# Kernel tuning notes

Measured on AMD Instinct MI355X. Metric: run time of the kernel, lower is better.

Reference implementation:

```python
import jax, jax.numpy as jnp
import numpy as np

N = 128   # system size (number of sequential RNN steps)
B = 8192  # batch of samples
H = 128   # hidden units per layer (units=[128,128])
D = 2     # input_dim (spin up/down one-hot)


def setup_inputs() -> dict:
    key = jax.random.key(0)
    ks = jax.random.split(key, 11)
    s = 1.0 / np.sqrt(H)  # torch nn.RNNCell/Linear default U(-1/sqrt(H), 1/sqrt(H))
    bits = jax.random.randint(ks[0], (N, B), 0, D)
    samples = jax.nn.one_hot(bits, D, dtype=jnp.float32)  # (N, B, D) one-hot spins
    u = lambda k, shp: jax.random.uniform(k, shp, jnp.float32, -s, s)
    return {
        "samples": samples,
        "W_ih0": u(ks[1], (H, D)), "b_ih0": u(ks[2], (H,)),
        "W_hh0": u(ks[3], (H, H)), "b_hh0": u(ks[4], (H,)),
        "W_ih1": u(ks[5], (H, H)), "b_ih1": u(ks[6], (H,)),
        "W_hh1": u(ks[7], (H, H)), "b_hh1": u(ks[8], (H,)),
        "W_dense": u(ks[9], (D, H)), "b_dense": u(ks[10], (D,)),
    }


def reference(samples, W_ih0, b_ih0, W_hh0, b_hh0,
              W_ih1, b_ih1, W_hh1, b_hh1, W_dense, b_dense):
    # Faithful jax port of RNN_wavefunction.log_prob:
    # p_t = <softmax(dense(h1_t)), s_t>; returns sum_t log p_t with shape (1, B).
    # For one-hot s_t, log(sum(prob*s_t)) == sum(s_t * log_softmax(logits)) (stable form).
    Bsz = samples.shape[1]
    # input at step t is the sampled spin from step t-1; zeros at t=0
    inputs = jnp.concatenate(
        [jnp.zeros((1, Bsz, D), samples.dtype), samples[:-1]], axis=0)
    h0 = jnp.zeros((Bsz, H), samples.dtype)
    h1 = jnp.zeros((Bsz, H), samples.dtype)

    def step(carry, xs):
        h0, h1 = carry
        x_t, s_t = xs  # x_t: (B, D) prev spin one-hot, s_t: (B, D) current spin
        # nn.RNNCell: h' = tanh(x W_ih^T + b_ih + h W_hh^T + b_hh)
        h0 = jnp.tanh(x_t @ W_ih0.T + b_ih0 + h0 @ W_hh0.T + b_hh0)
        h1 = jnp.tanh(h0 @ W_ih1.T + b_ih1 + h1 @ W_hh1.T + b_hh1)
        logits = h1 @ W_dense.T + b_dense           # (B, 2)
        logp = jax.nn.log_softmax(logits, axis=-1)
        lp_t = jnp.sum(logp * s_t, axis=-1)          # (B,) = log p(s_t)
        return (h0, h1), lp_t

    _, lps = jax.lax.scan(step, (h0, h1), (inputs, samples))  # lps: (N, B)
    return jnp.sum(lps, axis=0, keepdims=True)  # (1, B), matches torch keepdim=True
```

## Files before the change

### kernel.cpp

```cpp
#include <hip/hip_runtime.h>
#include <hip/hip_bf16.h>


#define NSTEP 128
#define BTOT  8192
#define HID   128
#define MB    16
#define NBLK  (BTOT / MB)
#define NTHR  256

typedef __attribute__((ext_vector_type(8))) short bf16x8;
typedef __attribute__((ext_vector_type(4))) float f32x4;

__device__ __forceinline__ short f2bf(float v) {
    unsigned u = __builtin_bit_cast(unsigned, v);
    u += 0x7FFFu + ((u >> 16) & 1u);
    return (short)(u >> 16);
}
__device__ __forceinline__ unsigned pk2bf(float a, float b) {
    unsigned ua = __builtin_bit_cast(unsigned, a);
    unsigned ub = __builtin_bit_cast(unsigned, b);
    ua += 0x7FFFu + ((ua >> 16) & 1u);
    ub += 0x7FFFu + ((ub >> 16) & 1u);
    return (ua >> 16) | (ub & 0xFFFF0000u);
}
__device__ __forceinline__ float fast_tanh(float x) {
    float e = __builtin_exp2f(x * 2.885390081777927f);
    float r = __builtin_amdgcn_rcpf(e + 1.0f);
    return 1.0f - 2.0f * r;
}

__global__ __launch_bounds__(NTHR, 2) void rnn_wf_kernel(
    const float* __restrict__ samples,
    const float* __restrict__ Wih0,
    const float* __restrict__ bih0,
    const float* __restrict__ Whh0,
    const float* __restrict__ bhh0,
    const float* __restrict__ Wih1,
    const float* __restrict__ bih1,
    const float* __restrict__ Whh1,
    const float* __restrict__ bhh1,
    const float* __restrict__ Wd,
    const float* __restrict__ bd,
    float* __restrict__ out)
{
    __shared__ short sH0[2][MB * HID];
    __shared__ short sH1[2][MB * HID];
    __shared__ unsigned sMask[NSTEP];

    const int tid  = threadIdx.x;
    const int b0   = blockIdx.x * MB;
    const int w    = tid >> 6;
    const int lane = tid & 63;
    const int q    = lane >> 4;
    const int c    = lane & 15;
    const int nb   = w * 32;

    for (int i = tid; i < MB * HID; i += NTHR) {
        sH0[0][i] = 0;
        sH1[0][i] = 0;
    }
    if (tid < NSTEP) {
        unsigned msk = 0;
        #pragma unroll
        for (int m = 0; m < MB; ++m) {
            float e1 = samples[((size_t)tid * BTOT + b0 + m) * 2 + 1];
            if (e1 > 0.5f) msk |= (1u << m);
        }
        sMask[tid] = msk;
    }

    bf16x8 fhh0[2][4], fih1[2][4], fhh1[2][4];
    #pragma unroll
    for (int nt = 0; nt < 2; ++nt) {
        const int nn = nb + nt * 16 + c;
        #pragma unroll
        for (int kb = 0; kb < 4; ++kb) {
            const int off = nn * HID + kb * 32 + q * 8;
            bf16x8 v0, v1, v2;
            #pragma unroll
            for (int j = 0; j < 8; ++j) {
                v0[j] = f2bf(Whh0[off + j]);
                v1[j] = f2bf(Wih1[off + j]);
                v2[j] = f2bf(Whh1[off + j]);
            }
            fhh0[nt][kb] = v0; fih1[nt][kb] = v1; fhh1[nt][kb] = v2;
        }
    }
    bf16x8 fwd[4];
    #pragma unroll
    for (int kb = 0; kb < 4; ++kb) {
        bf16x8 v;
        #pragma unroll
        for (int j = 0; j < 8; ++j)
            v[j] = (c < 2) ? f2bf(Wd[c * HID + kb * 32 + q * 8 + j]) : (short)0;
        fwd[kb] = v;
    }
    float pA[2][4], pB[2][4], b0v[2][4], b1v[2][4];
    #pragma unroll
    for (int nt = 0; nt < 2; ++nt)
        #pragma unroll
        for (int r = 0; r < 4; ++r) {
            const int n = nb + nt * 16 + q * 4 + r;
            const float bb = bih0[n] + bhh0[n];
            b0v[nt][r] = bb;
            pA[nt][r]  = bb + Wih0[n * 2 + 0];
            pB[nt][r]  = bb + Wih0[n * 2 + 1];
            b1v[nt][r] = bih1[n] + bhh1[n];
        }
    const float bd0 = bd[0], bd1 = bd[1];

    int ra[4];
    #pragma unroll
    for (int kb = 0; kb < 4; ++kb)
        ra[kb] = c * HID + (((kb * 4 + q) ^ (c & 7)) << 3);
    int wa[2];
    #pragma unroll
    for (int nt = 0; nt < 2; ++nt)
        wa[nt] = c * HID + ((((w << 2) + (nt << 1) + (q >> 1)) ^ (c & 7)) << 3)
               + ((q & 1) << 2);

    __syncthreads();

    float lp = 0.0f;
    int cur = 0;

    for (int t = 0; t < NSTEP; ++t) {
        const short* h0c = sH0[cur];
        short*       h0n = sH0[cur ^ 1];
        const short* h1c = sH1[cur];
        short*       h1n = sH1[cur ^ 1];

        const unsigned mPrev = (t > 0) ? sMask[t - 1] : 0u;
        const bool bm = (mPrev >> c) & 1u;
        const bool first = (t == 0);

        f32x4 acc0[2], acc1[2], accL = {0.f, 0.f, 0.f, 0.f};
        #pragma unroll
        for (int nt = 0; nt < 2; ++nt)
            #pragma unroll
            for (int r = 0; r < 4; ++r) {
                acc0[nt][r] = first ? b0v[nt][r] : (bm ? pB[nt][r] : pA[nt][r]);
                acc1[nt][r] = b1v[nt][r];
            }

        #pragma unroll
        for (int kb = 0; kb < 4; ++kb) {
            bf16x8 b0f = *reinterpret_cast<const bf16x8*>(&h0c[ra[kb]]);
            bf16x8 b1f = *reinterpret_cast<const bf16x8*>(&h1c[ra[kb]]);
            acc0[0] = __builtin_amdgcn_mfma_f32_16x16x32_bf16(fhh0[0][kb], b0f, acc0[0], 0, 0, 0);
            acc0[1] = __builtin_amdgcn_mfma_f32_16x16x32_bf16(fhh0[1][kb], b0f, acc0[1], 0, 0, 0);
            acc1[0] = __builtin_amdgcn_mfma_f32_16x16x32_bf16(fhh1[0][kb], b1f, acc1[0], 0, 0, 0);
            acc1[1] = __builtin_amdgcn_mfma_f32_16x16x32_bf16(fhh1[1][kb], b1f, acc1[1], 0, 0, 0);
            accL    = __builtin_amdgcn_mfma_f32_16x16x32_bf16(fwd[kb],     b1f, accL,    0, 0, 0);
        }

        if (t > 0) {
            const float l0 = accL[0] + bd0, l1 = accL[1] + bd1;
            const float lc = bm ? l1 : l0;
            const float lo = bm ? l0 : l1;
            const float ed = __builtin_exp2f((lo - lc) * 1.4426950408889634f);
            lp -= 0.6931471805599453f * __builtin_log2f(1.0f + ed);
        }

        #pragma unroll
        for (int nt = 0; nt < 2; ++nt) {
            const float t0 = fast_tanh(acc0[nt][0]);
            const float t1 = fast_tanh(acc0[nt][1]);
            const float t2 = fast_tanh(acc0[nt][2]);
            const float t3 = fast_tanh(acc0[nt][3]);
            const unsigned long long v =
                (unsigned long long)pk2bf(t0, t1) |
                ((unsigned long long)pk2bf(t2, t3) << 32);
            *reinterpret_cast<unsigned long long*>(&h0n[wa[nt]]) = v;
        }
        __syncthreads();

        #pragma unroll
        for (int kb = 0; kb < 4; ++kb) {
            bf16x8 bnf = *reinterpret_cast<const bf16x8*>(&h0n[ra[kb]]);
            acc1[0] = __builtin_amdgcn_mfma_f32_16x16x32_bf16(fih1[0][kb], bnf, acc1[0], 0, 0, 0);
            acc1[1] = __builtin_amdgcn_mfma_f32_16x16x32_bf16(fih1[1][kb], bnf, acc1[1], 0, 0, 0);
        }
        #pragma unroll
        for (int nt = 0; nt < 2; ++nt) {
            const float t0 = fast_tanh(acc1[nt][0]);
            const float t1 = fast_tanh(acc1[nt][1]);
            const float t2 = fast_tanh(acc1[nt][2]);
            const float t3 = fast_tanh(acc1[nt][3]);
            const unsigned long long v =
                (unsigned long long)pk2bf(t0, t1) |
                ((unsigned long long)pk2bf(t2, t3) << 32);
            *reinterpret_cast<unsigned long long*>(&h1n[wa[nt]]) = v;
        }
        __syncthreads();

        cur ^= 1;
    }

    {
        const short* h1f = sH1[cur];
        f32x4 accF = {0.f, 0.f, 0.f, 0.f};
        #pragma unroll
        for (int kb = 0; kb < 4; ++kb) {
            bf16x8 b1f = *reinterpret_cast<const bf16x8*>(&h1f[ra[kb]]);
            accF = __builtin_amdgcn_mfma_f32_16x16x32_bf16(fwd[kb], b1f, accF, 0, 0, 0);
        }
        const bool bm = (sMask[NSTEP - 1] >> c) & 1u;
        const float l0 = accF[0] + bd0, l1 = accF[1] + bd1;
        const float lc = bm ? l1 : l0;
        const float lo = bm ? l0 : l1;
        const float ed = __builtin_exp2f((lo - lc) * 1.4426950408889634f);
        lp -= 0.6931471805599453f * __builtin_log2f(1.0f + ed);
    }

    if (tid < 16)
        out[b0 + tid] = lp;
}

extern "C" void kernel_launch(void* const* d_in, const int* in_sizes, int n_in,
                              void* d_out, int out_size, void* d_ws, size_t ws_size,
                              hipStream_t stream) {
    rnn_wf_kernel<<<NBLK, NTHR, 0, stream>>>(
        (const float*)d_in[0],
        (const float*)d_in[1],
        (const float*)d_in[2],
        (const float*)d_in[3],
        (const float*)d_in[4],
        (const float*)d_in[5],
        (const float*)d_in[6],
        (const float*)d_in[7],
        (const float*)d_in[8],
        (const float*)d_in[9],
        (const float*)d_in[10],
        (float*)d_out);
}
```

Measured before the change: 294.5 us.

## Skew the two RNN layers by one step to halve barriers per step

Restructures the recurrence so layer 1 at step t-1 is computed in the same phase as layer 0 at step t. Both read the already-published h0/h1 buffers, which leaves one __syncthreads per step instead of two. A prologue and epilogue handle the skewed first and last steps. The change also packs tanh into two-wide vectors, broadens the LDS swizzle XOR to the full column index, and drops the zero-initialisation of the hidden buffers by seeding step 0 from the bias. The price is extra code and more live registers per step.

```diff
diff --git a/kernel.cpp b/kernel.cpp
--- a/kernel.cpp
+++ b/kernel.cpp
@@ -11,6 +11,8 @@
 
 typedef __attribute__((ext_vector_type(8))) short bf16x8;
 typedef __attribute__((ext_vector_type(4))) float f32x4;
+typedef __attribute__((ext_vector_type(2))) float f32x2;
+typedef __attribute__((ext_vector_type(2))) unsigned uint32x2;
 
 __device__ __forceinline__ short f2bf(float v) {
     unsigned u = __builtin_bit_cast(unsigned, v);
@@ -24,10 +26,16 @@
     ub += 0x7FFFu + ((ub >> 16) & 1u);
     return (ua >> 16) | (ub & 0xFFFF0000u);
 }
-__device__ __forceinline__ float fast_tanh(float x) {
-    float e = __builtin_exp2f(x * 2.885390081777927f);
-    float r = __builtin_amdgcn_rcpf(e + 1.0f);
-    return 1.0f - 2.0f * r;
+__device__ __forceinline__ f32x2 tanh2(f32x2 x) {
+    f32x2 z = x * 2.885390081777927f;
+    f32x2 e;
+    e.x = __builtin_exp2f(z.x);
+    e.y = __builtin_exp2f(z.y);
+    f32x2 d = e + 1.0f;
+    f32x2 r;
+    r.x = __builtin_amdgcn_rcpf(d.x);
+    r.y = __builtin_amdgcn_rcpf(d.y);
+    return r * -2.0f + 1.0f;
 }
 
 __global__ __launch_bounds__(NTHR, 2) void rnn_wf_kernel(
@@ -56,10 +64,6 @@
     const int c    = lane & 15;
     const int nb   = w * 32;
 
-    for (int i = tid; i < MB * HID; i += NTHR) {
-        sH0[0][i] = 0;
-        sH1[0][i] = 0;
-    }
     if (tid < NSTEP) {
         unsigned msk = 0;
         #pragma unroll
@@ -96,122 +100,144 @@
             v[j] = (c < 2) ? f2bf(Wd[c * HID + kb * 32 + q * 8 + j]) : (short)0;
         fwd[kb] = v;
     }
-    float pA[2][4], pB[2][4], b0v[2][4], b1v[2][4];
-    #pragma unroll
-    for (int nt = 0; nt < 2; ++nt)
-        #pragma unroll
-        for (int r = 0; r < 4; ++r) {
-            const int n = nb + nt * 16 + q * 4 + r;
-            const float bb = bih0[n] + bhh0[n];
-            b0v[nt][r] = bb;
-            pA[nt][r]  = bb + Wih0[n * 2 + 0];
-            pB[nt][r]  = bb + Wih0[n * 2 + 1];
-            b1v[nt][r] = bih1[n] + bhh1[n];
-        }
-    const float bd0 = bd[0], bd1 = bd[1];
+    f32x4 pA0, pA1, pB0, pB1, b0v0, b0v1, b1v0, b1v1;
+    #pragma unroll
+    for (int r = 0; r < 4; ++r) {
+        const int n0 = nb + q * 4 + r;
+        const int n1 = n0 + 16;
+        const float bb0 = bih0[n0] + bhh0[n0];
+        const float bb1 = bih0[n1] + bhh0[n1];
+        b0v0[r] = bb0;                    b0v1[r] = bb1;
+        pA0[r] = bb0 + Wih0[n0 * 2 + 0];  pA1[r] = bb1 + Wih0[n1 * 2 + 0];
+        pB0[r] = bb0 + Wih0[n0 * 2 + 1];  pB1[r] = bb1 + Wih0[n1 * 2 + 1];
+        b1v0[r] = bih1[n0] + bhh1[n0];    b1v1[r] = bih1[n1] + bhh1[n1];
+    }
+    const f32x4 bdv = {bd[0], bd[1], 0.f, 0.f};
 
     int ra[4];
     #pragma unroll
     for (int kb = 0; kb < 4; ++kb)
-        ra[kb] = c * HID + (((kb * 4 + q) ^ (c & 7)) << 3);
-    int wa[2];
-    #pragma unroll
-    for (int nt = 0; nt < 2; ++nt)
-        wa[nt] = c * HID + ((((w << 2) + (nt << 1) + (q >> 1)) ^ (c & 7)) << 3)
-               + ((q & 1) << 2);
-
-    __syncthreads();
+        ra[kb] = c * HID + (((kb * 4 + q) ^ c) << 3);
+    int wa0 = c * HID + (((4 * w + (q >> 1)) ^ c) << 3) + ((q & 1) << 2);
+    int wa1 = c * HID + (((4 * w + 2 + (q >> 1)) ^ c) << 3) + ((q & 1) << 2);
 
     float lp = 0.0f;
-    int cur = 0;
-
-    for (int t = 0; t < NSTEP; ++t) {
-        const short* h0c = sH0[cur];
-        short*       h0n = sH0[cur ^ 1];
-        const short* h1c = sH1[cur];
-        short*       h1n = sH1[cur ^ 1];
-
-        const unsigned mPrev = (t > 0) ? sMask[t - 1] : 0u;
-        const bool bm = (mPrev >> c) & 1u;
-        const bool first = (t == 0);
-
-        f32x4 acc0[2], acc1[2], accL = {0.f, 0.f, 0.f, 0.f};
-        #pragma unroll
-        for (int nt = 0; nt < 2; ++nt)
-            #pragma unroll
-            for (int r = 0; r < 4; ++r) {
-                acc0[nt][r] = first ? b0v[nt][r] : (bm ? pB[nt][r] : pA[nt][r]);
-                acc1[nt][r] = b1v[nt][r];
-            }
-
-        #pragma unroll
-        for (int kb = 0; kb < 4; ++kb) {
-            bf16x8 b0f = *reinterpret_cast<const bf16x8*>(&h0c[ra[kb]]);
-            bf16x8 b1f = *reinterpret_cast<const bf16x8*>(&h1c[ra[kb]]);
-            acc0[0] = __builtin_amdgcn_mfma_f32_16x16x32_bf16(fhh0[0][kb], b0f, acc0[0], 0, 0, 0);
-            acc0[1] = __builtin_amdgcn_mfma_f32_16x16x32_bf16(fhh0[1][kb], b0f, acc0[1], 0, 0, 0);
-            acc1[0] = __builtin_amdgcn_mfma_f32_16x16x32_bf16(fhh1[0][kb], b1f, acc1[0], 0, 0, 0);
-            acc1[1] = __builtin_amdgcn_mfma_f32_16x16x32_bf16(fhh1[1][kb], b1f, acc1[1], 0, 0, 0);
-            accL    = __builtin_amdgcn_mfma_f32_16x16x32_bf16(fwd[kb],     b1f, accL,    0, 0, 0);
-        }
-
-        if (t > 0) {
-            const float l0 = accL[0] + bd0, l1 = accL[1] + bd1;
-            const float lc = bm ? l1 : l0;
-            const float lo = bm ? l0 : l1;
-            const float ed = __builtin_exp2f((lo - lc) * 1.4426950408889634f);
-            lp -= 0.6931471805599453f * __builtin_log2f(1.0f + ed);
-        }
-
-        #pragma unroll
-        for (int nt = 0; nt < 2; ++nt) {
-            const float t0 = fast_tanh(acc0[nt][0]);
-            const float t1 = fast_tanh(acc0[nt][1]);
-            const float t2 = fast_tanh(acc0[nt][2]);
-            const float t3 = fast_tanh(acc0[nt][3]);
-            const unsigned long long v =
-                (unsigned long long)pk2bf(t0, t1) |
-                ((unsigned long long)pk2bf(t2, t3) << 32);
-            *reinterpret_cast<unsigned long long*>(&h0n[wa[nt]]) = v;
-        }
-        __syncthreads();
-
-        #pragma unroll
-        for (int kb = 0; kb < 4; ++kb) {
-            bf16x8 bnf = *reinterpret_cast<const bf16x8*>(&h0n[ra[kb]]);
-            acc1[0] = __builtin_amdgcn_mfma_f32_16x16x32_bf16(fih1[0][kb], bnf, acc1[0], 0, 0, 0);
-            acc1[1] = __builtin_amdgcn_mfma_f32_16x16x32_bf16(fih1[1][kb], bnf, acc1[1], 0, 0, 0);
-        }
-        #pragma unroll
-        for (int nt = 0; nt < 2; ++nt) {
-            const float t0 = fast_tanh(acc1[nt][0]);
-            const float t1 = fast_tanh(acc1[nt][1]);
-            const float t2 = fast_tanh(acc1[nt][2]);
-            const float t3 = fast_tanh(acc1[nt][3]);
-            const unsigned long long v =
-                (unsigned long long)pk2bf(t0, t1) |
-                ((unsigned long long)pk2bf(t2, t3) << 32);
-            *reinterpret_cast<unsigned long long*>(&h1n[wa[nt]]) = v;
-        }
-        __syncthreads();
-
-        cur ^= 1;
-    }
-
-    {
-        const short* h1f = sH1[cur];
-        f32x4 accF = {0.f, 0.f, 0.f, 0.f};
-        #pragma unroll
-        for (int kb = 0; kb < 4; ++kb) {
-            bf16x8 b1f = *reinterpret_cast<const bf16x8*>(&h1f[ra[kb]]);
-            accF = __builtin_amdgcn_mfma_f32_16x16x32_bf16(fwd[kb], b1f, accF, 0, 0, 0);
-        }
-        const bool bm = (sMask[NSTEP - 1] >> c) & 1u;
-        const float l0 = accF[0] + bd0, l1 = accF[1] + bd1;
-        const float lc = bm ? l1 : l0;
-        const float lo = bm ? l0 : l1;
+    bool bmPrev = false;
+
+    auto storeH = [&](short* buf, const f32x4& a0, const f32x4& a1) {
+        f32x2 t00 = tanh2((f32x2){a0[0], a0[1]});
+        f32x2 t01 = tanh2((f32x2){a0[2], a0[3]});
+        f32x2 t10 = tanh2((f32x2){a1[0], a1[1]});
+        f32x2 t11 = tanh2((f32x2){a1[2], a1[3]});
+        uint32x2 v0 = {pk2bf(t00.x, t00.y), pk2bf(t01.x, t01.y)};
+        uint32x2 v1 = {pk2bf(t10.x, t10.y), pk2bf(t11.x, t11.y)};
+        *reinterpret_cast<uint32x2*>(&buf[wa0]) = v0;
+        *reinterpret_cast<uint32x2*>(&buf[wa1]) = v1;
+    };
+    auto lpAdd = [&](const f32x4& aL, bool bit) {
+        const float l0 = aL[0], l1 = aL[1];
+        const float lc = bit ? l1 : l0;
+        const float lo = bit ? l0 : l1;
         const float ed = __builtin_exp2f((lo - lc) * 1.4426950408889634f);
         lp -= 0.6931471805599453f * __builtin_log2f(1.0f + ed);
+    };
+
+    __syncthreads();
+    storeH(sH0[1], b0v0, b0v1);
+    __syncthreads();
+
+    {
+        const bool bmIn = (sMask[0] >> c) & 1u;
+        bf16x8 f0[4];
+        #pragma unroll
+        for (int kb = 0; kb < 4; ++kb)
+            f0[kb] = *reinterpret_cast<const bf16x8*>(&sH0[1][ra[kb]]);
+        f32x4 a00 = bmIn ? pB0 : pA0;
+        f32x4 a01 = bmIn ? pB1 : pA1;
+        f32x4 a10 = b1v0, a11 = b1v1;
+        #pragma unroll
+        for (int kb = 0; kb < 4; ++kb) {
+            a00 = __builtin_amdgcn_mfma_f32_16x16x32_bf16(fhh0[0][kb], f0[kb], a00, 0, 0, 0);
+            a01 = __builtin_amdgcn_mfma_f32_16x16x32_bf16(fhh0[1][kb], f0[kb], a01, 0, 0, 0);
+            a10 = __builtin_amdgcn_mfma_f32_16x16x32_bf16(fih1[0][kb], f0[kb], a10, 0, 0, 0);
+            a11 = __builtin_amdgcn_mfma_f32_16x16x32_bf16(fih1[1][kb], f0[kb], a11, 0, 0, 0);
+        }
+        storeH(sH0[0], a00, a01);
+        storeH(sH1[0], a10, a11);
+        bmPrev = bmIn;
+        __syncthreads();
+    }
+
+    auto stepMain = [&](int i, const short* r0, const short* r1,
+                        short* w0b, short* w1b) {
+        const bool bmIn = (sMask[i - 1] >> c) & 1u;
+        bf16x8 f0[4], f1[4];
+        #pragma unroll
+        for (int kb = 0; kb < 4; ++kb) {
+            f0[kb] = *reinterpret_cast<const bf16x8*>(&r0[ra[kb]]);
+            f1[kb] = *reinterpret_cast<const bf16x8*>(&r1[ra[kb]]);
+        }
+        f32x4 a00 = bmIn ? pB0 : pA0;
+        f32x4 a01 = bmIn ? pB1 : pA1;
+        f32x4 a10 = b1v0, a11 = b1v1;
+        f32x4 aL  = bdv;
+        #pragma unroll
+        for (int kb = 0; kb < 4; ++kb) {
+            a00 = __builtin_amdgcn_mfma_f32_16x16x32_bf16(fhh0[0][kb], f0[kb], a00, 0, 0, 0);
+            a01 = __builtin_amdgcn_mfma_f32_16x16x32_bf16(fhh0[1][kb], f0[kb], a01, 0, 0, 0);
+            a10 = __builtin_amdgcn_mfma_f32_16x16x32_bf16(fhh1[0][kb], f1[kb], a10, 0, 0, 0);
+            a11 = __builtin_amdgcn_mfma_f32_16x16x32_bf16(fhh1[1][kb], f1[kb], a11, 0, 0, 0);
+            aL  = __builtin_amdgcn_mfma_f32_16x16x32_bf16(fwd[kb],     f1[kb], aL,  0, 0, 0);
+        }
+        #pragma unroll
+        for (int kb = 0; kb < 4; ++kb) {
+            a10 = __builtin_amdgcn_mfma_f32_16x16x32_bf16(fih1[0][kb], f0[kb], a10, 0, 0, 0);
+            a11 = __builtin_amdgcn_mfma_f32_16x16x32_bf16(fih1[1][kb], f0[kb], a11, 0, 0, 0);
+        }
+        lpAdd(aL, bmPrev);
+        bmPrev = bmIn;
+        storeH(w0b, a00, a01);
+        storeH(w1b, a10, a11);
+        __syncthreads();
+    };
+
+    for (int i = 2; i < NSTEP; i += 2) {
+        stepMain(i,     sH0[0], sH1[0], sH0[1], sH1[1]);
+        stepMain(i + 1, sH0[1], sH1[1], sH0[0], sH1[0]);
+    }
+
+    {
+        bf16x8 f0[4], f1[4];
+        #pragma unroll
+        for (int kb = 0; kb < 4; ++kb) {
+            f0[kb] = *reinterpret_cast<const bf16x8*>(&sH0[0][ra[kb]]);
+            f1[kb] = *reinterpret_cast<const bf16x8*>(&sH1[0][ra[kb]]);
+        }
+        f32x4 a10 = b1v0, a11 = b1v1;
+        f32x4 aL  = bdv;
+        #pragma unroll
+        for (int kb = 0; kb < 4; ++kb) {
+            a10 = __builtin_amdgcn_mfma_f32_16x16x32_bf16(fhh1[0][kb], f1[kb], a10, 0, 0, 0);
+            a11 = __builtin_amdgcn_mfma_f32_16x16x32_bf16(fhh1[1][kb], f1[kb], a11, 0, 0, 0);
+            aL  = __builtin_amdgcn_mfma_f32_16x16x32_bf16(fwd[kb],     f1[kb], aL,  0, 0, 0);
+        }
+        #pragma unroll
+        for (int kb = 0; kb < 4; ++kb) {
+            a10 = __builtin_amdgcn_mfma_f32_16x16x32_bf16(fih1[0][kb], f0[kb], a10, 0, 0, 0);
+            a11 = __builtin_amdgcn_mfma_f32_16x16x32_bf16(fih1[1][kb], f0[kb], a11, 0, 0, 0);
+        }
+        lpAdd(aL, bmPrev);
+        storeH(sH1[1], a10, a11);
+        __syncthreads();
+    }
+    {
+        f32x4 aL = bdv;
+        #pragma unroll
+        for (int kb = 0; kb < 4; ++kb) {
+            bf16x8 f1 = *reinterpret_cast<const bf16x8*>(&sH1[1][ra[kb]]);
+            aL = __builtin_amdgcn_mfma_f32_16x16x32_bf16(fwd[kb], f1, aL, 0, 0, 0);
+        }
+        lpAdd(aL, (sMask[NSTEP - 1] >> c) & 1u);
     }
 
     if (tid < 16)
```

New measurement: 263.2 us. -10.6%, faster.
